# Optimization experiments

Hardware: AMD Instinct MI355X
Metric: run time of the kernel (lower is better)

## Reference

```python
import jax, jax.numpy as jnp
import numpy as np

CONT_FIELD = 13
CATE_FIELD = 26
VOCAB = 100000
EMB_DIM = 40
ATTN_DIM = 8
BATCH = 4096


def setup_inputs() -> dict:
    key = jax.random.key(0)
    ks = jax.random.split(key, 8)
    conts = jax.random.uniform(ks[0], (BATCH, CONT_FIELD), dtype=jnp.float32)
    cates = jax.random.randint(ks[1], (BATCH, CATE_FIELD), 0, VOCAB, dtype=jnp.int64)
    combs = jax.random.normal(ks[2], (BATCH, 1), dtype=jnp.float32)
    a = np.square(3.0 / (CATE_FIELD * EMB_DIM))
    emb_table = jax.random.uniform(ks[3], (VOCAB, EMB_DIM), minval=-a, maxval=a, dtype=jnp.float32)
    attn_W = jax.random.normal(ks[4], (ATTN_DIM, EMB_DIM), dtype=jnp.float32) * 0.1
    attn_b = jnp.zeros((ATTN_DIM,), dtype=jnp.float32)
    proj_W = jax.random.normal(ks[5], (1, ATTN_DIM), dtype=jnp.float32) * 0.3
    fc_W = jax.random.normal(ks[6], (1, EMB_DIM), dtype=jnp.float32) * 0.1
    fc_b = jnp.zeros((1,), dtype=jnp.float32)
    return {"conts": conts, "cates": cates, "combs": combs, "emb_table": emb_table,
            "attn_W": attn_W, "attn_b": attn_b, "proj_W": proj_W, "fc_W": fc_W, "fc_b": fc_b}


def reference(conts, cates, combs, emb_table, attn_W, attn_b, proj_W, fc_W, fc_b):
    # continuous fields use fixed embedding rows 0..CONT_FIELD-1 scaled by value
    cont_emb = emb_table[jnp.arange(CONT_FIELD)][None, :, :] * conts[:, :, None]  # (B, 13, D)
    cate_emb = emb_table[cates]                                                   # (B, 26, D)
    x = jnp.concatenate([cont_emb, cate_emb], axis=1)                             # (B, 39, D)
    row, col = jnp.triu_indices(CONT_FIELD + CATE_FIELD, k=1)                     # 741 pairs
    ewp = x[:, row, :] * x[:, col, :]                                             # (B, 741, D)
    h = jax.nn.relu(jnp.einsum('bpd,ad->bpa', ewp, attn_W) + attn_b)              # (B, 741, 8)
    logits = jnp.einsum('bpa,oa->bpo', h, proj_W)                                 # (B, 741, 1)
    attn = jax.nn.softmax(logits, axis=1)                                         # softmax over pairs
    pooled = jnp.sum(attn * ewp, axis=1)                                          # (B, D)
    out = jax.nn.sigmoid(pooled @ fc_W.T + fc_b)                                  # (B, 1)
    return out
```

## Files before the change

### kernel.cpp

```cpp
#include <hip/hip_runtime.h>
#include <math.h>

#define NF 39
#define CONT_F 13
#define CATE_F 26
#define EMB_D 40
#define VOCAB 100000
#define NCH 9
#define ROW_B 80
#define CH_B  3120

typedef __attribute__((ext_vector_type(8))) short short8;
typedef __attribute__((ext_vector_type(4))) float f32x4;

__device__ __forceinline__ unsigned pack_bf16x2_trunc(float a, float b) {
    return (__float_as_uint(b) & 0xFFFF0000u) | (__float_as_uint(a) >> 16);
}

__global__ __launch_bounds__(192, 3)
void afm_mfma_kernel(const float* __restrict__ conts,
                     const int*   __restrict__ cates,
                     const float* __restrict__ emb,
                     const float* __restrict__ attn_W,
                     const float* __restrict__ attn_b,
                     const float* __restrict__ proj_W,
                     const float* __restrict__ fc_W,
                     const float* __restrict__ fc_b,
                     float* __restrict__ out)
{
    __shared__ __attribute__((aligned(16))) unsigned short Xb[NF * EMB_D];
    __shared__ __attribute__((aligned(16))) unsigned short Aall[NCH * NF * EMB_D];
    __shared__ __attribute__((aligned(16))) float zero16[4];
    __shared__ float reds[3], redg[3];

    const int tid = threadIdx.x;
    const int row = blockIdx.x;

    if (tid < 4) zero16[tid] = 0.f;

    {
        const float4* emb4 = (const float4*)emb;
        unsigned* XbW = (unsigned*)Xb;
        unsigned* AW  = (unsigned*)Aall;
        for (int t = tid; t < NF * 10; t += 192) {
            const int f = t / 10, q = t % 10;
            float4 v;
            if (f < CONT_F) {
                v = emb4[f * 10 + q];
                const float cs = conts[row * CONT_F + f];
                v.x *= cs; v.y *= cs; v.z *= cs; v.w *= cs;
            } else {
                unsigned u = (unsigned)cates[row * CATE_F + (f - CONT_F)];
                if (u >= (unsigned)VOCAB) u = 0;
                v = emb4[u * 10 + q];
            }
            const int wofs = f * 20 + q * 2;
            *(uint2*)&XbW[wofs] = make_uint2(pack_bf16x2_trunc(v.x, v.y),
                                             pack_bf16x2_trunc(v.z, v.w));
            #pragma unroll
            for (int c = 0; c < NCH; ++c) {
                const float4 wv = (c < 8) ? ((const float4*)attn_W)[c * 10 + q]
                                          : ((const float4*)fc_W)[q];
                *(uint2*)&AW[c * 780 + wofs] =
                    make_uint2(pack_bf16x2_trunc(v.x * wv.x, v.y * wv.y),
                               pack_bf16x2_trunc(v.z * wv.z, v.w * wv.w));
            }
        }
    }
    __syncthreads();

    const int wid  = tid >> 6;
    const int lane = tid & 63;
    const int l15  = lane & 15;
    const int quad = lane >> 4;

    int rA = wid * 16 + l15; if (rA > NF - 1) rA = NF - 1;

    const char* XbP = (const char*)Xb;
    const char* AP  = (const char*)Aall;
    const char* ZP  = (const char*)zero16;

    short8 b0[3], b1[3];
    #pragma unroll
    for (int nt = 0; nt < 3; ++nt) {
        if (nt >= wid) {
            int rB = nt * 16 + l15; if (rB > NF - 1) rB = NF - 1;
            b0[nt] = *(const short8*)(XbP + rB * ROW_B + quad * 16);
            b1[nt] = *(const short8*)((quad == 0) ? (XbP + rB * ROW_B + 64) : ZP);
        }
    }

    float pj[8], bb[8];
    #pragma unroll
    for (int a = 0; a < 8; ++a) { pj[a] = proj_W[a]; bb[a] = attn_b[a]; }

    float lacc[3][4] = {{0}};
    float gv[3][4];

    #pragma unroll
    for (int c = 0; c < NCH; ++c) {
        const char* aRow = AP + c * CH_B + rA * ROW_B;
        const short8 a0 = *(const short8*)(aRow + quad * 16);
        const short8 a1 = *(const short8*)((quad == 0) ? (aRow + 64) : ZP);
        f32x4 z[3];
        #pragma unroll
        for (int nt = 0; nt < 3; ++nt) {
            if (nt >= wid) {
                f32x4 t = {0.f, 0.f, 0.f, 0.f};
                t = __builtin_amdgcn_mfma_f32_16x16x32_bf16(a0, b0[nt], t, 0, 0, 0);
                t = __builtin_amdgcn_mfma_f32_16x16x32_bf16(a1, b1[nt], t, 0, 0, 0);
                z[nt] = t;
            }
        }
        #pragma unroll
        for (int nt = 0; nt < 3; ++nt) {
            if (nt >= wid) {
                #pragma unroll
                for (int r = 0; r < 4; ++r) {
                    if (c < 8)
                        lacc[nt][r] = fmaf(pj[c], fmaxf(z[nt][r] + bb[c], 0.f),
                                           lacc[nt][r]);
                    else
                        gv[nt][r] = z[nt][r];
                }
            }
        }
    }

    float s = 0.f, gs = 0.f;
    #pragma unroll
    for (int nt = 0; nt < 3; ++nt) {
        if (nt >= wid) {
            #pragma unroll
            for (int r = 0; r < 4; ++r) {
                const int i = wid * 16 + quad * 4 + r;
                const int j = nt * 16 + l15;
                if (i < j && j < NF) {
                    const float e = __expf(lacc[nt][r]);
                    s += e;
                    gs = fmaf(e, gv[nt][r], gs);
                }
            }
        }
    }
    #pragma unroll
    for (int off = 32; off; off >>= 1) {
        s  += __shfl_xor(s, off);
        gs += __shfl_xor(gs, off);
    }
    if (lane == 0) { reds[wid] = s; redg[wid] = gs; }
    __syncthreads();

    if (tid == 0) {
        const float S = reds[0] + reds[1] + reds[2];
        const float G = redg[0] + redg[1] + redg[2];
        const float zf = G / S + fc_b[0];
        out[row] = 1.f / (1.f + __expf(-zf));
    }
}

extern "C" void kernel_launch(void* const* d_in, const int* in_sizes, int n_in,
                              void* d_out, int out_size, void* d_ws, size_t ws_size,
                              hipStream_t stream) {
    const float* conts  = (const float*)d_in[0];
    const int*   cates  = (const int*)  d_in[1];
    const float* emb    = (const float*)d_in[3];
    const float* attn_W = (const float*)d_in[4];
    const float* attn_b = (const float*)d_in[5];
    const float* proj_W = (const float*)d_in[6];
    const float* fc_W   = (const float*)d_in[7];
    const float* fc_b   = (const float*)d_in[8];
    float* out = (float*)d_out;

    const int batch = in_sizes[0] / CONT_F;
    afm_mfma_kernel<<<batch, 192, 0, stream>>>(
        conts, cates, emb, attn_W, attn_b, proj_W, fc_W, fc_b, out);
}
```

Measured before the change: 103.6 us.

## Switch pair-interaction MFMA from bf16 to scaled fp8 with balanced wave tiles

Stores the embedding rows and the weight-premultiplied rows in shared memory as fp8 e4m3 after scaling by 2^20, and uses fp8 16x16x32 MFMA with the result rescaled by 2^-40. This halves LDS footprint and packing cost and raises the launch-bounds occupancy hint. The three upper-triangular tile pairs are redistributed so each wave computes exactly two output tiles instead of 3/2/1. The fp8 quantization risks accuracy loss relative to the bf16 path.

Result: slower. 108.1 us (+4.4%).

```diff
diff --git a/kernel.cpp b/kernel.cpp
--- a/kernel.cpp
+++ b/kernel.cpp
@@ -7,63 +7,82 @@
 #define EMB_D 40
 #define VOCAB 100000
 #define NCH 9
-#define ROW_B 80
-#define CH_B  3120
+#define ROW_B 40
+#define CH_B (NF * ROW_B)
+#define CH_W (NF * 10)
 
-typedef __attribute__((ext_vector_type(8))) short short8;
 typedef __attribute__((ext_vector_type(4))) float f32x4;
 
-__device__ __forceinline__ unsigned pack_bf16x2_trunc(float a, float b) {
-    return (__float_as_uint(b) & 0xFFFF0000u) | (__float_as_uint(a) >> 16);
+__device__ __forceinline__ unsigned f32_to_e4m3_sw(float f) {
+    unsigned u = __float_as_uint(f);
+    unsigned s = (u >> 24) & 0x80u;
+    int e = (int)((u >> 23) & 0xFFu) - 127;
+    unsigned m = u & 0x7FFFFFu;
+    if (e < -6) return s;
+    unsigned m3 = (m + 0x7FFFFu + ((m >> 20) & 1u)) >> 20;
+    if (m3 >= 8u) { m3 -= 8u; ++e; }
+    if (e > 8) { e = 8; m3 = 6u; }
+    return s | ((unsigned)(e + 7) << 3) | m3;
 }
 
-__global__ __launch_bounds__(192, 3)
-void afm_mfma_kernel(const float* __restrict__ conts,
-                     const int*   __restrict__ cates,
-                     const float* __restrict__ emb,
-                     const float* __restrict__ attn_W,
-                     const float* __restrict__ attn_b,
-                     const float* __restrict__ proj_W,
-                     const float* __restrict__ fc_W,
-                     const float* __restrict__ fc_b,
-                     float* __restrict__ out)
+template <bool HI>
+__device__ __forceinline__ unsigned cvt2_fp8(float a, float b, unsigned old) {
+#if __has_builtin(__builtin_amdgcn_cvt_pk_fp8_f32)
+    return __builtin_amdgcn_cvt_pk_fp8_f32(a, b, old, HI);
+#else
+    unsigned p = f32_to_e4m3_sw(a) | (f32_to_e4m3_sw(b) << 8);
+    return HI ? ((old & 0x0000FFFFu) | (p << 16)) : ((old & 0xFFFF0000u) | p);
+#endif
+}
+
+__device__ __forceinline__ int clamp_row(int r) { return r > NF - 1 ? NF - 1 : r; }
+
+__global__ __launch_bounds__(192, 6)
+void afm_fp8_kernel(const float* __restrict__ conts,
+                    const int*   __restrict__ cates,
+                    const float* __restrict__ emb,
+                    const float* __restrict__ attn_W,
+                    const float* __restrict__ attn_b,
+                    const float* __restrict__ proj_W,
+                    const float* __restrict__ fc_W,
+                    const float* __restrict__ fc_b,
+                    float* __restrict__ out)
 {
-    __shared__ __attribute__((aligned(16))) unsigned short Xb[NF * EMB_D];
-    __shared__ __attribute__((aligned(16))) unsigned short Aall[NCH * NF * EMB_D];
-    __shared__ __attribute__((aligned(16))) float zero16[4];
+    __shared__ __attribute__((aligned(16))) unsigned char Xb[NF * ROW_B];
+    __shared__ __attribute__((aligned(16))) unsigned char Aall[NCH * CH_B];
     __shared__ float reds[3], redg[3];
 
     const int tid = threadIdx.x;
     const int row = blockIdx.x;
 
-    if (tid < 4) zero16[tid] = 0.f;
-
     {
         const float4* emb4 = (const float4*)emb;
         unsigned* XbW = (unsigned*)Xb;
         unsigned* AW  = (unsigned*)Aall;
+        const float SC = 1048576.0f;
         for (int t = tid; t < NF * 10; t += 192) {
             const int f = t / 10, q = t % 10;
             float4 v;
             if (f < CONT_F) {
                 v = emb4[f * 10 + q];
-                const float cs = conts[row * CONT_F + f];
+                const float cs = conts[row * CONT_F + f] * SC;
                 v.x *= cs; v.y *= cs; v.z *= cs; v.w *= cs;
             } else {
                 unsigned u = (unsigned)cates[row * CATE_F + (f - CONT_F)];
                 if (u >= (unsigned)VOCAB) u = 0;
                 v = emb4[u * 10 + q];
+                v.x *= SC; v.y *= SC; v.z *= SC; v.w *= SC;
             }
-            const int wofs = f * 20 + q * 2;
-            *(uint2*)&XbW[wofs] = make_uint2(pack_bf16x2_trunc(v.x, v.y),
-                                             pack_bf16x2_trunc(v.z, v.w));
+            unsigned xw = cvt2_fp8<false>(v.x, v.y, 0u);
+            xw = cvt2_fp8<true>(v.z, v.w, xw);
+            XbW[f * 10 + q] = xw;
             #pragma unroll
             for (int c = 0; c < NCH; ++c) {
                 const float4 wv = (c < 8) ? ((const float4*)attn_W)[c * 10 + q]
                                           : ((const float4*)fc_W)[q];
-                *(uint2*)&AW[c * 780 + wofs] =
-                    make_uint2(pack_bf16x2_trunc(v.x * wv.x, v.y * wv.y),
-                               pack_bf16x2_trunc(v.z * wv.z, v.w * wv.w));
+                unsigned aw = cvt2_fp8<false>(v.x * wv.x, v.y * wv.y, 0u);
+                aw = cvt2_fp8<true>(v.z * wv.z, v.w * wv.w, aw);
+                AW[c * CH_W + f * 10 + q] = aw;
             }
         }
     }
@@ -74,72 +93,69 @@
     const int l15  = lane & 15;
     const int quad = lane >> 4;
 
-    int rA = wid * 16 + l15; if (rA > NF - 1) rA = NF - 1;
+    const int TM[3][2] = {{0, 0}, {0, 1}, {1, 2}};
+    const int TN[3][2] = {{0, 1}, {2, 1}, {2, 2}};
+    const int mt0 = TM[wid][0], mt1 = TM[wid][1];
+    const int nt0 = TN[wid][0], nt1 = TN[wid][1];
 
-    const char* XbP = (const char*)Xb;
-    const char* AP  = (const char*)Aall;
-    const char* ZP  = (const char*)zero16;
+    const int rA0 = clamp_row(mt0 * 16 + l15);
+    const int rA1 = clamp_row(mt1 * 16 + l15);
+    const int rB0 = clamp_row(nt0 * 16 + l15);
+    const int rB1 = clamp_row(nt1 * 16 + l15);
 
-    short8 b0[3], b1[3];
-    #pragma unroll
-    for (int nt = 0; nt < 3; ++nt) {
-        if (nt >= wid) {
-            int rB = nt * 16 + l15; if (rB > NF - 1) rB = NF - 1;
-            b0[nt] = *(const short8*)(XbP + rB * ROW_B + quad * 16);
-            b1[nt] = *(const short8*)((quad == 0) ? (XbP + rB * ROW_B + 64) : ZP);
-        }
-    }
+    const unsigned char* XbP = Xb;
+    long b0[2], b1[2];
+    b0[0] = *(const long*)(XbP + rB0 * ROW_B + quad * 8);
+    b1[0] = (quad == 0) ? *(const long*)(XbP + rB0 * ROW_B + 32) : 0L;
+    b0[1] = *(const long*)(XbP + rB1 * ROW_B + quad * 8);
+    b1[1] = (quad == 0) ? *(const long*)(XbP + rB1 * ROW_B + 32) : 0L;
 
     float pj[8], bb[8];
     #pragma unroll
     for (int a = 0; a < 8; ++a) { pj[a] = proj_W[a]; bb[a] = attn_b[a]; }
 
-    float lacc[3][4] = {{0}};
-    float gv[3][4];
+    const float INV = 0x1p-40f;
+    float lacc[2][4] = {{0.f, 0.f, 0.f, 0.f}, {0.f, 0.f, 0.f, 0.f}};
+    float gv[2][4];
 
     #pragma unroll
     for (int c = 0; c < NCH; ++c) {
-        const char* aRow = AP + c * CH_B + rA * ROW_B;
-        const short8 a0 = *(const short8*)(aRow + quad * 16);
-        const short8 a1 = *(const short8*)((quad == 0) ? (aRow + 64) : ZP);
-        f32x4 z[3];
-        #pragma unroll
-        for (int nt = 0; nt < 3; ++nt) {
-            if (nt >= wid) {
-                f32x4 t = {0.f, 0.f, 0.f, 0.f};
-                t = __builtin_amdgcn_mfma_f32_16x16x32_bf16(a0, b0[nt], t, 0, 0, 0);
-                t = __builtin_amdgcn_mfma_f32_16x16x32_bf16(a1, b1[nt], t, 0, 0, 0);
-                z[nt] = t;
+        const unsigned char* aB = Aall + c * CH_B;
+        const long a00 = *(const long*)(aB + rA0 * ROW_B + quad * 8);
+        const long a01 = (quad == 0) ? *(const long*)(aB + rA0 * ROW_B + 32) : 0L;
+        const long a10 = *(const long*)(aB + rA1 * ROW_B + quad * 8);
+        const long a11 = (quad == 0) ? *(const long*)(aB + rA1 * ROW_B + 32) : 0L;
+        f32x4 z0 = {0.f, 0.f, 0.f, 0.f};
+        f32x4 z1 = {0.f, 0.f, 0.f, 0.f};
+        z0 = __builtin_amdgcn_mfma_f32_16x16x32_fp8_fp8(a00, b0[0], z0, 0, 0, 0);
+        z0 = __builtin_amdgcn_mfma_f32_16x16x32_fp8_fp8(a01, b1[0], z0, 0, 0, 0);
+        z1 = __builtin_amdgcn_mfma_f32_16x16x32_fp8_fp8(a10, b0[1], z1, 0, 0, 0);
+        z1 = __builtin_amdgcn_mfma_f32_16x16x32_fp8_fp8(a11, b1[1], z1, 0, 0, 0);
+        if (c < 8) {
+            #pragma unroll
+            for (int r = 0; r < 4; ++r) {
+                lacc[0][r] = fmaf(pj[c], fmaxf(fmaf(z0[r], INV, bb[c]), 0.f), lacc[0][r]);
+                lacc[1][r] = fmaf(pj[c], fmaxf(fmaf(z1[r], INV, bb[c]), 0.f), lacc[1][r]);
             }
-        }
-        #pragma unroll
-        for (int nt = 0; nt < 3; ++nt) {
-            if (nt >= wid) {
-                #pragma unroll
-                for (int r = 0; r < 4; ++r) {
-                    if (c < 8)
-                        lacc[nt][r] = fmaf(pj[c], fmaxf(z[nt][r] + bb[c], 0.f),
-                                           lacc[nt][r]);
-                    else
-                        gv[nt][r] = z[nt][r];
-                }
-            }
+        } else {
+            #pragma unroll
+            for (int r = 0; r < 4; ++r) { gv[0][r] = z0[r]; gv[1][r] = z1[r]; }
         }
     }
 
     float s = 0.f, gs = 0.f;
     #pragma unroll
-    for (int nt = 0; nt < 3; ++nt) {
-        if (nt >= wid) {
-            #pragma unroll
-            for (int r = 0; r < 4; ++r) {
-                const int i = wid * 16 + quad * 4 + r;
-                const int j = nt * 16 + l15;
-                if (i < j && j < NF) {
-                    const float e = __expf(lacc[nt][r]);
-                    s += e;
-                    gs = fmaf(e, gv[nt][r], gs);
-                }
+    for (int t = 0; t < 2; ++t) {
+        const int mt = (t == 0) ? mt0 : mt1;
+        const int nt = (t == 0) ? nt0 : nt1;
+        #pragma unroll
+        for (int r = 0; r < 4; ++r) {
+            const int i = mt * 16 + quad * 4 + r;
+            const int j = nt * 16 + l15;
+            if (i < j && j < NF) {
+                const float e = __expf(lacc[t][r]);
+                s += e;
+                gs = fmaf(e, gv[t][r], gs);
             }
         }
     }
@@ -153,7 +169,7 @@
 
     if (tid == 0) {
         const float S = reds[0] + reds[1] + reds[2];
-        const float G = redg[0] + redg[1] + redg[2];
+        const float G = (redg[0] + redg[1] + redg[2]) * INV;
         const float zf = G / S + fc_b[0];
         out[row] = 1.f / (1.f + __expf(-zf));
     }
@@ -173,6 +189,6 @@
     float* out = (float*)d_out;
 
     const int batch = in_sizes[0] / CONT_F;
-    afm_mfma_kernel<<<batch, 192, 0, stream>>>(
+    afm_fp8_kernel<<<batch, 192, 0, stream>>>(
         conts, cates, emb, attn_W, attn_b, proj_W, fc_W, fc_b, out);
 }
```
